# Kernel optimization log

Hardware: AMD Instinct MI355X
Metric: run time of the kernel (lower is better)

## Reference

```python
import jax, jax.numpy as jnp
import numpy as np

IN_DIM = 1024
OUT_DIM = 1024
BATCH = 256
NUM_OBJS = 100


def setup_inputs() -> dict:
    key = jax.random.key(0)
    k1, k2, k3, k4, k5 = jax.random.split(key, 5)
    stdv = 1.0 / np.sqrt(OUT_DIM)
    feature = jax.random.normal(k1, (BATCH, NUM_OBJS, IN_DIM), dtype=jnp.float32)
    graph = jax.random.randint(k2, (BATCH, NUM_OBJS, NUM_OBJS), 0, 2, dtype=jnp.int32)
    weight = jax.random.uniform(k3, (IN_DIM, OUT_DIM), dtype=jnp.float32, minval=-stdv, maxval=stdv)
    # DotProduct(in_dim, in_dim, out_dim): project both operands to hidden dim, batched dot product
    wq = jax.random.uniform(k4, (IN_DIM, OUT_DIM), dtype=jnp.float32, minval=-stdv, maxval=stdv)
    wk = jax.random.uniform(k5, (IN_DIM, OUT_DIM), dtype=jnp.float32, minval=-stdv, maxval=stdv)
    return {"feature": feature, "graph": graph, "weight": weight, "wq": wq, "wk": wk}


def reference(feature, graph, weight, wq, wk):
    # output = feature @ W                              [B, N, out_dim]
    output = jnp.einsum("bni,io->bno", feature, weight)
    # alpha = dot_product(feature, feature)             [B, N, N]
    q = jnp.einsum("bni,io->bno", feature, wq)
    k = jnp.einsum("bni,io->bno", feature, wk)
    alpha = jnp.einsum("bno,bmo->bnm", q, k)
    # relu scores, mask by adjacency, softmax over dim=1
    alpha = jnp.maximum(alpha, 0.0) * (graph != 0).astype(alpha.dtype)
    alpha = jax.nn.softmax(alpha, axis=1)
    # aggregate
    return jnp.einsum("bnm,bmo->bno", alpha, output)
```

## Files before the change

### kernel.cpp

```cpp
#include <hip/hip_runtime.h>
#include <cstdint>
#include <cstddef>

#define NOBJ 100

typedef __attribute__((ext_vector_type(8))) short short8;
typedef __attribute__((ext_vector_type(4))) float f32x4;

typedef const __attribute__((address_space(1))) void* gas_cptr;
typedef __attribute__((address_space(3))) void* las_ptr;

__device__ __forceinline__ void gload_lds16(const void* g, void* l) {
  __builtin_amdgcn_global_load_lds((gas_cptr)g, (las_ptr)l, 16, 0, 0);
}

__device__ __forceinline__ unsigned short bf16_rtne(float x) {
  unsigned u = __builtin_bit_cast(unsigned, x);
  unsigned r = u + 0x7FFFu + ((u >> 16) & 1u);
  return (unsigned short)(r >> 16);
}
__device__ __forceinline__ float bf16_to_f32(unsigned short h) {
  unsigned u = ((unsigned)h) << 16;
  return __builtin_bit_cast(float, u);
}

__global__ __launch_bounds__(256)
void split_ew(const float* __restrict__ in, unsigned short* __restrict__ hi,
              unsigned short* __restrict__ lo, long long n8) {
  for (long long u = (long long)blockIdx.x * 256 + threadIdx.x; u < n8;
       u += (long long)gridDim.x * 256) {
    const float4* p = (const float4*)(in + u * 8);
    float4 v0 = p[0], v1 = p[1];
    float x[8] = {v0.x, v0.y, v0.z, v0.w, v1.x, v1.y, v1.z, v1.w};
    unsigned h[8], l[8];
#pragma unroll
    for (int j = 0; j < 8; ++j) {
      h[j] = bf16_rtne(x[j]);
      l[j] = bf16_rtne(x[j] - bf16_to_f32((unsigned short)h[j]));
    }
    uint4 hv, lv;
    hv.x = h[0] | (h[1] << 16); hv.y = h[2] | (h[3] << 16);
    hv.z = h[4] | (h[5] << 16); hv.w = h[6] | (h[7] << 16);
    lv.x = l[0] | (l[1] << 16); lv.y = l[2] | (l[3] << 16);
    lv.z = l[4] | (l[5] << 16); lv.w = l[6] | (l[7] << 16);
    *(uint4*)(hi + u * 8) = hv;
    *(uint4*)(lo + u * 8) = lv;
  }
}

__global__ __launch_bounds__(256)
void split_tr(const float* __restrict__ W, unsigned short* __restrict__ thi,
              unsigned short* __restrict__ tlo) {
  __shared__ float tile[32][33];
  const int r0 = blockIdx.y * 32, c0 = blockIdx.x * 32;
  const int tx = threadIdx.x & 31, ty = threadIdx.x >> 5;
  for (int rr = ty; rr < 32; rr += 8)
    tile[rr][tx] = W[(size_t)(r0 + rr) * 1024 + c0 + tx];
  __syncthreads();
  for (int cc = ty; cc < 32; cc += 8) {
    float x = tile[tx][cc];
    unsigned short h = bf16_rtne(x);
    unsigned short l = bf16_rtne(x - bf16_to_f32(h));
    size_t o = (size_t)(c0 + cc) * 1024 + r0 + tx;
    thi[o] = h;
    tlo[o] = l;
  }
}

template<int EPI>
__global__ __launch_bounds__(256)
void gemm_mfma3(const unsigned short* __restrict__ Ah, const unsigned short* __restrict__ Al,
                const unsigned short* __restrict__ Bh, const unsigned short* __restrict__ Bl,
                unsigned short* __restrict__ Ch, unsigned short* __restrict__ Cl,
                int M, int N, int K) {
  __shared__ unsigned short s_ah[4096], s_al[4096], s_bh[4096], s_bl[4096];
  const int t = threadIdx.x;
  const int wid = t >> 6, lane = t & 63;
  const int wr = wid >> 1, wc = wid & 1;
  const int lrow = lane & 15, q = lane >> 4;
  const int m0 = blockIdx.y * 128, n0 = blockIdx.x * 128;

  const int srow = t >> 2;
  const int skch = (t & 3) ^ ((t >> 3) & 3);
  const unsigned short* gAh = Ah + (size_t)(m0 + srow) * K + skch * 8;
  const unsigned short* gAl = Al + (size_t)(m0 + srow) * K + skch * 8;
  const unsigned short* gBh = Bh + (size_t)(n0 + srow) * K + skch * 8;
  const unsigned short* gBl = Bl + (size_t)(n0 + srow) * K + skch * 8;
  const size_t rstep = (size_t)64 * K;
  unsigned short* dA0  = &s_ah[wid * 512];
  unsigned short* dA1  = &s_ah[wid * 512 + 2048];
  unsigned short* dAl0 = &s_al[wid * 512];
  unsigned short* dAl1 = &s_al[wid * 512 + 2048];
  unsigned short* dB0  = &s_bh[wid * 512];
  unsigned short* dB1  = &s_bh[wid * 512 + 2048];
  unsigned short* dBl0 = &s_bl[wid * 512];
  unsigned short* dBl1 = &s_bl[wid * 512 + 2048];

  const int fq = (q ^ ((lrow >> 1) & 3)) * 8;

  f32x4 acc[4][4];
#pragma unroll
  for (int i = 0; i < 4; ++i)
#pragma unroll
    for (int j = 0; j < 4; ++j) acc[i][j] = (f32x4){0.f, 0.f, 0.f, 0.f};

  for (int kc = 0; kc < K; kc += 32) {
    gload_lds16(gAh + kc, dA0);
    gload_lds16(gAh + kc + rstep, dA1);
    gload_lds16(gAl + kc, dAl0);
    gload_lds16(gAl + kc + rstep, dAl1);
    gload_lds16(gBh + kc, dB0);
    gload_lds16(gBh + kc + rstep, dB1);
    gload_lds16(gBl + kc, dBl0);
    gload_lds16(gBl + kc + rstep, dBl1);
    __syncthreads();

    short8 a_h[4], a_l[4];
#pragma unroll
    for (int i = 0; i < 4; ++i) {
      const int ra = (wr * 64 + i * 16 + lrow) * 32 + fq;
      a_h[i] = *(const short8*)&s_ah[ra];
      a_l[i] = *(const short8*)&s_al[ra];
    }
#pragma unroll
    for (int j = 0; j < 4; ++j) {
      const int rb = (wc * 64 + j * 16 + lrow) * 32 + fq;
      short8 b_h = *(const short8*)&s_bh[rb];
      short8 b_l = *(const short8*)&s_bl[rb];
#pragma unroll
      for (int i = 0; i < 4; ++i) {
        acc[i][j] = __builtin_amdgcn_mfma_f32_16x16x32_bf16(a_h[i], b_h, acc[i][j], 0, 0, 0);
        acc[i][j] = __builtin_amdgcn_mfma_f32_16x16x32_bf16(a_h[i], b_l, acc[i][j], 0, 0, 0);
        acc[i][j] = __builtin_amdgcn_mfma_f32_16x16x32_bf16(a_l[i], b_h, acc[i][j], 0, 0, 0);
      }
    }
    __syncthreads();
  }

#pragma unroll
  for (int i = 0; i < 4; ++i) {
    const int row0 = m0 + wr * 64 + i * 16 + q * 4;
#pragma unroll
    for (int j = 0; j < 4; ++j) {
      const int col = n0 + wc * 64 + j * 16 + lrow;
      unsigned short h[4];
#pragma unroll
      for (int r = 0; r < 4; ++r) h[r] = bf16_rtne(acc[i][j][r]);
      if (EPI == 0) {
#pragma unroll
        for (int r = 0; r < 4; ++r) {
          const size_t o = (size_t)(row0 + r) * N + col;
          Ch[o] = h[r];
          Cl[o] = bf16_rtne(acc[i][j][r] - bf16_to_f32(h[r]));
        }
      } else if (EPI == 1) {
        const unsigned bb = (unsigned)row0 / 100u;
        const unsigned ml = (unsigned)row0 - bb * 100u;
        uint2 hv;
        hv.x = (unsigned)h[0] | ((unsigned)h[1] << 16);
        hv.y = (unsigned)h[2] | ((unsigned)h[3] << 16);
        *(uint2*)(Ch + ((size_t)bb * 1024 + col) * 128 + ml) = hv;
      } else {
        unsigned short l[4];
#pragma unroll
        for (int r = 0; r < 4; ++r) l[r] = bf16_rtne(acc[i][j][r] - bf16_to_f32(h[r]));
        uint2 hv, lv;
        hv.x = (unsigned)h[0] | ((unsigned)h[1] << 16);
        hv.y = (unsigned)h[2] | ((unsigned)h[3] << 16);
        lv.x = (unsigned)l[0] | ((unsigned)l[1] << 16);
        lv.y = (unsigned)l[2] | ((unsigned)l[3] << 16);
        *(uint2*)(Ch + (size_t)col * 1024 + row0) = hv;
        *(uint2*)(Cl + (size_t)col * 1024 + row0) = lv;
      }
    }
  }
}

__global__ __launch_bounds__(256)
void attn_scores_mfma(const unsigned short* __restrict__ Qh, const unsigned short* __restrict__ Ql,
                      const unsigned short* __restrict__ Xh, const unsigned short* __restrict__ Xl,
                      const int* __restrict__ graph, float* __restrict__ S) {
  __shared__ unsigned short s_ah[4096], s_al[4096], s_bh[4096], s_bl[4096];
  __shared__ float s[NOBJ * NOBJ];
  const int t = threadIdx.x;
  const int wid = t >> 6, lane = t & 63;
  const int wr = wid >> 1, wc = wid & 1;
  const int lrow = lane & 15, q = lane >> 4;
  const int bb = blockIdx.x;

  const int srow = t >> 2;
  const int skch = (t & 3) ^ ((t >> 3) & 3);
  const int r0c = srow;
  const int r1c = (srow + 64) < NOBJ ? (srow + 64) : (NOBJ - 1);
  const size_t base = (size_t)bb * NOBJ * 1024;
  const unsigned short* gQh0 = Qh + base + (size_t)r0c * 1024 + skch * 8;
  const unsigned short* gQh1 = Qh + base + (size_t)r1c * 1024 + skch * 8;
  const unsigned short* gQl0 = Ql + base + (size_t)r0c * 1024 + skch * 8;
  const unsigned short* gQl1 = Ql + base + (size_t)r1c * 1024 + skch * 8;
  const unsigned short* gXh0 = Xh + base + (size_t)r0c * 1024 + skch * 8;
  const unsigned short* gXh1 = Xh + base + (size_t)r1c * 1024 + skch * 8;
  const unsigned short* gXl0 = Xl + base + (size_t)r0c * 1024 + skch * 8;
  const unsigned short* gXl1 = Xl + base + (size_t)r1c * 1024 + skch * 8;
  unsigned short* dA0  = &s_ah[wid * 512];
  unsigned short* dA1  = &s_ah[wid * 512 + 2048];
  unsigned short* dAl0 = &s_al[wid * 512];
  unsigned short* dAl1 = &s_al[wid * 512 + 2048];
  unsigned short* dB0  = &s_bh[wid * 512];
  unsigned short* dB1  = &s_bh[wid * 512 + 2048];
  unsigned short* dBl0 = &s_bl[wid * 512];
  unsigned short* dBl1 = &s_bl[wid * 512 + 2048];

  const int fq = (q ^ ((lrow >> 1) & 3)) * 8;

  f32x4 acc[4][4];
#pragma unroll
  for (int i = 0; i < 4; ++i)
#pragma unroll
    for (int j = 0; j < 4; ++j) acc[i][j] = (f32x4){0.f, 0.f, 0.f, 0.f};

  for (int kc = 0; kc < 1024; kc += 32) {
    gload_lds16(gQh0 + kc, dA0);
    gload_lds16(gQh1 + kc, dA1);
    gload_lds16(gQl0 + kc, dAl0);
    gload_lds16(gQl1 + kc, dAl1);
    gload_lds16(gXh0 + kc, dB0);
    gload_lds16(gXh1 + kc, dB1);
    gload_lds16(gXl0 + kc, dBl0);
    gload_lds16(gXl1 + kc, dBl1);
    __syncthreads();

    short8 a_h[4], a_l[4];
#pragma unroll
    for (int i = 0; i < 4; ++i) {
      const int ra = (wr * 64 + i * 16 + lrow) * 32 + fq;
      a_h[i] = *(const short8*)&s_ah[ra];
      a_l[i] = *(const short8*)&s_al[ra];
    }
#pragma unroll
    for (int j = 0; j < 4; ++j) {
      const int rb = (wc * 64 + j * 16 + lrow) * 32 + fq;
      short8 b_h = *(const short8*)&s_bh[rb];
      short8 b_l = *(const short8*)&s_bl[rb];
#pragma unroll
      for (int i = 0; i < 4; ++i) {
        acc[i][j] = __builtin_amdgcn_mfma_f32_16x16x32_bf16(a_h[i], b_h, acc[i][j], 0, 0, 0);
        acc[i][j] = __builtin_amdgcn_mfma_f32_16x16x32_bf16(a_h[i], b_l, acc[i][j], 0, 0, 0);
        acc[i][j] = __builtin_amdgcn_mfma_f32_16x16x32_bf16(a_l[i], b_h, acc[i][j], 0, 0, 0);
      }
    }
    __syncthreads();
  }

  const int* gb = graph + (size_t)bb * NOBJ * NOBJ;
#pragma unroll
  for (int i = 0; i < 4; ++i) {
    const int row0 = wr * 64 + i * 16 + q * 4;
#pragma unroll
    for (int j = 0; j < 4; ++j) {
      const int col = wc * 64 + j * 16 + lrow;
      if (col < NOBJ) {
#pragma unroll
        for (int r = 0; r < 4; ++r) {
          const int n = row0 + r;
          if (n < NOBJ) {
            float v = acc[i][j][r];
            v = v > 0.f ? v : 0.f;
            s[n * NOBJ + col] = (gb[n * NOBJ + col] != 0) ? v : 0.f;
          }
        }
      }
    }
  }
  __syncthreads();

  if (t < NOBJ) {
    const int m = t;
    float mx = 0.f;
    for (int n = 0; n < NOBJ; ++n) mx = fmaxf(mx, s[n * NOBJ + m]);
    float sum = 0.f;
    for (int n = 0; n < NOBJ; ++n) {
      const float e = expf(s[n * NOBJ + m] - mx);
      s[n * NOBJ + m] = e;
      sum += e;
    }
    const float inv = 1.f / sum;
    for (int n = 0; n < NOBJ; ++n) s[n * NOBJ + m] *= inv;
  }
  __syncthreads();

  float* Sb = S + (size_t)bb * NOBJ * NOBJ;
  for (int idx = t; idx < NOBJ * NOBJ; idx += 256) Sb[idx] = s[idx];
}

__global__ __launch_bounds__(256)
void attn_agg_mfma(const float* __restrict__ S, const unsigned short* __restrict__ opT,
                   float* __restrict__ out) {
  __shared__ unsigned short shi[128 * 128];
  __shared__ unsigned short slo[128 * 128];
  __shared__ unsigned short bt[64 * 128];
  const int t = threadIdx.x;
  const int wid = t >> 6, lane = t & 63;
  const int wr = wid >> 1, wc = wid & 1;
  const int lrow = lane & 15, q = lane >> 4;
  const int bb = blockIdx.y, o0 = blockIdx.x * 64;

#pragma unroll
  for (int p = 0; p < 4; ++p) {
    const int u = p * 256 + t;
    const int row = u >> 4, sl = u & 15;
    const int sp = sl ^ (row & 7);
    gload_lds16(opT + ((size_t)(bb * 1024 + o0 + row)) * 128 + sp * 8,
                bt + (p * 256 + wid * 64) * 8);
  }

  {
    unsigned* z1 = (unsigned*)shi;
    unsigned* z2 = (unsigned*)slo;
    for (int idx = t; idx < 8192; idx += 256) { z1[idx] = 0u; z2[idx] = 0u; }
  }
  __syncthreads();

  const float* Sb = S + (size_t)bb * NOBJ * NOBJ;
  for (int idx = t; idx < NOBJ * NOBJ / 4; idx += 256) {
    const float4 v = ((const float4*)Sb)[idx];
    const int lin = idx * 4, n = lin / NOBJ, m = lin - n * NOBJ;
    const float x[4] = {v.x, v.y, v.z, v.w};
    unsigned short h[4], l[4];
#pragma unroll
    for (int e = 0; e < 4; ++e) {
      h[e] = bf16_rtne(x[e]);
      l[e] = bf16_rtne(x[e] - bf16_to_f32(h[e]));
    }
    const int byte = ((n * 128 + m) * 2) ^ ((n & 7) << 4);
    uint2 hv, lv;
    hv.x = (unsigned)h[0] | ((unsigned)h[1] << 16);
    hv.y = (unsigned)h[2] | ((unsigned)h[3] << 16);
    lv.x = (unsigned)l[0] | ((unsigned)l[1] << 16);
    lv.y = (unsigned)l[2] | ((unsigned)l[3] << 16);
    *(uint2*)((char*)shi + byte) = hv;
    *(uint2*)((char*)slo + byte) = lv;
  }
  __syncthreads();

  f32x4 acc[4][2];
#pragma unroll
  for (int i = 0; i < 4; ++i)
#pragma unroll
    for (int j = 0; j < 2; ++j) acc[i][j] = (f32x4){0.f, 0.f, 0.f, 0.f};

#pragma unroll
  for (int ks = 0; ks < 4; ++ks) {
    short8 ah[4], al[4], bv[2];
#pragma unroll
    for (int i = 0; i < 4; ++i) {
      const int row = wr * 64 + i * 16 + lrow;
      const int byte = row * 256 + (((ks * 4 + q) ^ (row & 7)) * 16);
      ah[i] = *(const short8*)((char*)shi + byte);
      al[i] = *(const short8*)((char*)slo + byte);
    }
#pragma unroll
    for (int j = 0; j < 2; ++j) {
      const int brow = wc * 32 + j * 16 + lrow;
      const int byte = brow * 256 + (((ks * 4 + q) ^ (brow & 7)) * 16);
      bv[j] = *(const short8*)((char*)bt + byte);
    }
#pragma unroll
    for (int i = 0; i < 4; ++i)
#pragma unroll
      for (int j = 0; j < 2; ++j) {
        acc[i][j] = __builtin_amdgcn_mfma_f32_16x16x32_bf16(ah[i], bv[j], acc[i][j], 0, 0, 0);
        acc[i][j] = __builtin_amdgcn_mfma_f32_16x16x32_bf16(al[i], bv[j], acc[i][j], 0, 0, 0);
      }
  }

#pragma unroll
  for (int i = 0; i < 4; ++i) {
    const int row0 = wr * 64 + i * 16 + q * 4;
#pragma unroll
    for (int j = 0; j < 2; ++j) {
      const int col = o0 + wc * 32 + j * 16 + lrow;
#pragma unroll
      for (int r = 0; r < 4; ++r) {
        const int n = row0 + r;
        if (n < NOBJ)
          out[((size_t)bb * NOBJ + n) * 1024 + col] = acc[i][j][r];
      }
    }
  }
}

extern "C" void kernel_launch(void* const* d_in, const int* in_sizes, int n_in,
                              void* d_out, int out_size, void* d_ws, size_t ws_size,
                              hipStream_t stream) {
  const float* feature = (const float*)d_in[0];
  const int*   graph   = (const int*)  d_in[1];
  const float* weight  = (const float*)d_in[2];
  const float* wq      = (const float*)d_in[3];
  const float* wk      = (const float*)d_in[4];
  float* out = (float*)d_out;

  const size_t NF = (size_t)25600 * 1024;
  const size_t OPT = (size_t)256 * 1024 * 128;
  const size_t W1 = (size_t)1024 * 1024;
  const size_t need = (2 * NF + OPT + 8 * W1) * 2 + (size_t)2560000 * 4;
  if (ws_size < need) return;

  unsigned short* qkhi  = (unsigned short*)d_ws;
  unsigned short* qklo  = qkhi + NF;
  unsigned short* opT   = qklo + NF;
  unsigned short* wthi  = opT + OPT;
  unsigned short* wtlo  = wthi + W1;
  unsigned short* m1thi = wtlo + W1;
  unsigned short* m1tlo = m1thi + W1;
  unsigned short* wqhi  = m1tlo + W1;
  unsigned short* wqlo  = wqhi + W1;
  unsigned short* wkhi  = wqlo + W1;
  unsigned short* wklo  = wkhi + W1;
  float* S = (float*)(wklo + W1);
  unsigned short* xhi = (unsigned short*)d_out;
  unsigned short* xlo = xhi + NF;

  const dim3 blk(256);
  split_ew<<<4096, blk, 0, stream>>>(feature, xhi, xlo, (long long)(NF / 8));
  split_ew<<<512, blk, 0, stream>>>(wq, wqhi, wqlo, (long long)(W1 / 8));
  split_ew<<<512, blk, 0, stream>>>(wk, wkhi, wklo, (long long)(W1 / 8));
  split_tr<<<dim3(32, 32), blk, 0, stream>>>(weight, wthi, wtlo);
  gemm_mfma3<2><<<dim3(8, 8), blk, 0, stream>>>(wqhi, wqlo, wkhi, wklo,
                                                m1thi, m1tlo, 1024, 1024, 1024);
  gemm_mfma3<1><<<dim3(8, 200), blk, 0, stream>>>(xhi, xlo, wthi, wtlo,
                                                  opT, nullptr, 25600, 1024, 1024);
  gemm_mfma3<0><<<dim3(8, 200), blk, 0, stream>>>(xhi, xlo, m1thi, m1tlo,
                                                  qkhi, qklo, 25600, 1024, 1024);
  attn_scores_mfma<<<dim3(256), blk, 0, stream>>>(qkhi, qklo, xhi, xlo, graph, S);
  attn_agg_mfma<<<dim3(16, 256), blk, 0, stream>>>(S, opT, out);
}
```

Measured before the change: 794.6 us.

## Switch split-precision from bf16 to fp16, merge projection GEMMs, widen score blocks

Every hi/lo split and MFMA moves from bf16 to fp16, using the hardware float-to-half conversion in place of manual bit rounding. The two big projection GEMMs (feature@W and feature@M1) become one launch of 3200 workgroups with a remapped block order, so tiles that share the same feature rows sit on nearby workgroups. The attention-score kernel goes to 512 threads with 8 waves, covering the 100 rows in one tile instead of two overlapping 64-row loads. The cost is fp16's narrower exponent range, which could overflow or underflow for some inputs.

```diff
diff --git a/kernel.cpp b/kernel.cpp
--- a/kernel.cpp
+++ b/kernel.cpp
@@ -4,7 +4,7 @@
 
 #define NOBJ 100
 
-typedef __attribute__((ext_vector_type(8))) short short8;
+typedef __attribute__((ext_vector_type(8))) _Float16 half8;
 typedef __attribute__((ext_vector_type(4))) float f32x4;
 
 typedef const __attribute__((address_space(1))) void* gas_cptr;
@@ -14,14 +14,14 @@
   __builtin_amdgcn_global_load_lds((gas_cptr)g, (las_ptr)l, 16, 0, 0);
 }
 
-__device__ __forceinline__ unsigned short bf16_rtne(float x) {
-  unsigned u = __builtin_bit_cast(unsigned, x);
-  unsigned r = u + 0x7FFFu + ((u >> 16) & 1u);
-  return (unsigned short)(r >> 16);
-}
-__device__ __forceinline__ float bf16_to_f32(unsigned short h) {
-  unsigned u = ((unsigned)h) << 16;
-  return __builtin_bit_cast(float, u);
+__device__ __forceinline__ unsigned short f16h(float x) {
+  return __builtin_bit_cast(unsigned short, (_Float16)x);
+}
+__device__ __forceinline__ void f16split(float x, unsigned& h, unsigned& l) {
+  _Float16 hh = (_Float16)x;
+  _Float16 ll = (_Float16)(x - (float)hh);
+  h = (unsigned)__builtin_bit_cast(unsigned short, hh);
+  l = (unsigned)__builtin_bit_cast(unsigned short, ll);
 }
 
 __global__ __launch_bounds__(256)
@@ -34,10 +34,7 @@
     float x[8] = {v0.x, v0.y, v0.z, v0.w, v1.x, v1.y, v1.z, v1.w};
     unsigned h[8], l[8];
 #pragma unroll
-    for (int j = 0; j < 8; ++j) {
-      h[j] = bf16_rtne(x[j]);
-      l[j] = bf16_rtne(x[j] - bf16_to_f32((unsigned short)h[j]));
-    }
+    for (int j = 0; j < 8; ++j) f16split(x[j], h[j], l[j]);
     uint4 hv, lv;
     hv.x = h[0] | (h[1] << 16); hv.y = h[2] | (h[3] << 16);
     hv.z = h[4] | (h[5] << 16); hv.w = h[6] | (h[7] << 16);
@@ -59,20 +56,18 @@
   __syncthreads();
   for (int cc = ty; cc < 32; cc += 8) {
     float x = tile[tx][cc];
-    unsigned short h = bf16_rtne(x);
-    unsigned short l = bf16_rtne(x - bf16_to_f32(h));
+    unsigned h, l;
+    f16split(x, h, l);
     size_t o = (size_t)(c0 + cc) * 1024 + r0 + tx;
-    thi[o] = h;
-    tlo[o] = l;
-  }
-}
-
-template<int EPI>
+    thi[o] = (unsigned short)h;
+    tlo[o] = (unsigned short)l;
+  }
+}
+
 __global__ __launch_bounds__(256)
-void gemm_mfma3(const unsigned short* __restrict__ Ah, const unsigned short* __restrict__ Al,
-                const unsigned short* __restrict__ Bh, const unsigned short* __restrict__ Bl,
-                unsigned short* __restrict__ Ch, unsigned short* __restrict__ Cl,
-                int M, int N, int K) {
+void gemm_m1(const unsigned short* __restrict__ Ah, const unsigned short* __restrict__ Al,
+             const unsigned short* __restrict__ Bh, const unsigned short* __restrict__ Bl,
+             unsigned short* __restrict__ Th, unsigned short* __restrict__ Tl) {
   __shared__ unsigned short s_ah[4096], s_al[4096], s_bh[4096], s_bl[4096];
   const int t = threadIdx.x;
   const int wid = t >> 6, lane = t & 63;
@@ -82,11 +77,11 @@
 
   const int srow = t >> 2;
   const int skch = (t & 3) ^ ((t >> 3) & 3);
-  const unsigned short* gAh = Ah + (size_t)(m0 + srow) * K + skch * 8;
-  const unsigned short* gAl = Al + (size_t)(m0 + srow) * K + skch * 8;
-  const unsigned short* gBh = Bh + (size_t)(n0 + srow) * K + skch * 8;
-  const unsigned short* gBl = Bl + (size_t)(n0 + srow) * K + skch * 8;
-  const size_t rstep = (size_t)64 * K;
+  const unsigned short* gAh = Ah + (size_t)(m0 + srow) * 1024 + skch * 8;
+  const unsigned short* gAl = Al + (size_t)(m0 + srow) * 1024 + skch * 8;
+  const unsigned short* gBh = Bh + (size_t)(n0 + srow) * 1024 + skch * 8;
+  const unsigned short* gBl = Bl + (size_t)(n0 + srow) * 1024 + skch * 8;
+  const size_t rstep = (size_t)64 * 1024;
   unsigned short* dA0  = &s_ah[wid * 512];
   unsigned short* dA1  = &s_ah[wid * 512 + 2048];
   unsigned short* dAl0 = &s_al[wid * 512];
@@ -95,7 +90,6 @@
   unsigned short* dB1  = &s_bh[wid * 512 + 2048];
   unsigned short* dBl0 = &s_bl[wid * 512];
   unsigned short* dBl1 = &s_bl[wid * 512 + 2048];
-
   const int fq = (q ^ ((lrow >> 1) & 3)) * 8;
 
   f32x4 acc[4][4];
@@ -104,7 +98,7 @@
 #pragma unroll
     for (int j = 0; j < 4; ++j) acc[i][j] = (f32x4){0.f, 0.f, 0.f, 0.f};
 
-  for (int kc = 0; kc < K; kc += 32) {
+  for (int kc = 0; kc < 1024; kc += 32) {
     gload_lds16(gAh + kc, dA0);
     gload_lds16(gAh + kc + rstep, dA1);
     gload_lds16(gAl + kc, dAl0);
@@ -114,24 +108,23 @@
     gload_lds16(gBl + kc, dBl0);
     gload_lds16(gBl + kc + rstep, dBl1);
     __syncthreads();
-
-    short8 a_h[4], a_l[4];
+    half8 a_h[4], a_l[4];
 #pragma unroll
     for (int i = 0; i < 4; ++i) {
       const int ra = (wr * 64 + i * 16 + lrow) * 32 + fq;
-      a_h[i] = *(const short8*)&s_ah[ra];
-      a_l[i] = *(const short8*)&s_al[ra];
+      a_h[i] = *(const half8*)&s_ah[ra];
+      a_l[i] = *(const half8*)&s_al[ra];
     }
 #pragma unroll
     for (int j = 0; j < 4; ++j) {
       const int rb = (wc * 64 + j * 16 + lrow) * 32 + fq;
-      short8 b_h = *(const short8*)&s_bh[rb];
-      short8 b_l = *(const short8*)&s_bl[rb];
+      half8 b_h = *(const half8*)&s_bh[rb];
+      half8 b_l = *(const half8*)&s_bl[rb];
 #pragma unroll
       for (int i = 0; i < 4; ++i) {
-        acc[i][j] = __builtin_amdgcn_mfma_f32_16x16x32_bf16(a_h[i], b_h, acc[i][j], 0, 0, 0);
-        acc[i][j] = __builtin_amdgcn_mfma_f32_16x16x32_bf16(a_h[i], b_l, acc[i][j], 0, 0, 0);
-        acc[i][j] = __builtin_amdgcn_mfma_f32_16x16x32_bf16(a_l[i], b_h, acc[i][j], 0, 0, 0);
+        acc[i][j] = __builtin_amdgcn_mfma_f32_16x16x32_f16(a_h[i], b_h, acc[i][j], 0, 0, 0);
+        acc[i][j] = __builtin_amdgcn_mfma_f32_16x16x32_f16(a_h[i], b_l, acc[i][j], 0, 0, 0);
+        acc[i][j] = __builtin_amdgcn_mfma_f32_16x16x32_f16(a_l[i], b_h, acc[i][j], 0, 0, 0);
       }
     }
     __syncthreads();
@@ -143,64 +136,46 @@
 #pragma unroll
     for (int j = 0; j < 4; ++j) {
       const int col = n0 + wc * 64 + j * 16 + lrow;
-      unsigned short h[4];
-#pragma unroll
-      for (int r = 0; r < 4; ++r) h[r] = bf16_rtne(acc[i][j][r]);
-      if (EPI == 0) {
-#pragma unroll
-        for (int r = 0; r < 4; ++r) {
-          const size_t o = (size_t)(row0 + r) * N + col;
-          Ch[o] = h[r];
-          Cl[o] = bf16_rtne(acc[i][j][r] - bf16_to_f32(h[r]));
-        }
-      } else if (EPI == 1) {
-        const unsigned bb = (unsigned)row0 / 100u;
-        const unsigned ml = (unsigned)row0 - bb * 100u;
-        uint2 hv;
-        hv.x = (unsigned)h[0] | ((unsigned)h[1] << 16);
-        hv.y = (unsigned)h[2] | ((unsigned)h[3] << 16);
-        *(uint2*)(Ch + ((size_t)bb * 1024 + col) * 128 + ml) = hv;
-      } else {
-        unsigned short l[4];
-#pragma unroll
-        for (int r = 0; r < 4; ++r) l[r] = bf16_rtne(acc[i][j][r] - bf16_to_f32(h[r]));
-        uint2 hv, lv;
-        hv.x = (unsigned)h[0] | ((unsigned)h[1] << 16);
-        hv.y = (unsigned)h[2] | ((unsigned)h[3] << 16);
-        lv.x = (unsigned)l[0] | ((unsigned)l[1] << 16);
-        lv.y = (unsigned)l[2] | ((unsigned)l[3] << 16);
-        *(uint2*)(Ch + (size_t)col * 1024 + row0) = hv;
-        *(uint2*)(Cl + (size_t)col * 1024 + row0) = lv;
-      }
+      unsigned h[4], l[4];
+#pragma unroll
+      for (int r = 0; r < 4; ++r) f16split(acc[i][j][r], h[r], l[r]);
+      uint2 hv, lv;
+      hv.x = h[0] | (h[1] << 16); hv.y = h[2] | (h[3] << 16);
+      lv.x = l[0] | (l[1] << 16); lv.y = l[2] | (l[3] << 16);
+      *(uint2*)(Th + (size_t)col * 1024 + row0) = hv;
+      *(uint2*)(Tl + (size_t)col * 1024 + row0) = lv;
     }
   }
 }
 
 __global__ __launch_bounds__(256)
-void attn_scores_mfma(const unsigned short* __restrict__ Qh, const unsigned short* __restrict__ Ql,
-                      const unsigned short* __restrict__ Xh, const unsigned short* __restrict__ Xl,
-                      const int* __restrict__ graph, float* __restrict__ S) {
+void proj_gemm(const unsigned short* __restrict__ Ah, const unsigned short* __restrict__ Al,
+               const unsigned short* __restrict__ Wh, const unsigned short* __restrict__ Wl,
+               const unsigned short* __restrict__ Mh, const unsigned short* __restrict__ Ml,
+               unsigned short* __restrict__ opT, unsigned short* __restrict__ qkh,
+               unsigned short* __restrict__ qkl) {
   __shared__ unsigned short s_ah[4096], s_al[4096], s_bh[4096], s_bl[4096];
-  __shared__ float s[NOBJ * NOBJ];
   const int t = threadIdx.x;
   const int wid = t >> 6, lane = t & 63;
   const int wr = wid >> 1, wc = wid & 1;
   const int lrow = lane & 15, q = lane >> 4;
-  const int bb = blockIdx.x;
+
+  const int bid  = blockIdx.x;
+  const int wgid = (bid & 7) * 400 + (bid >> 3);
+  const int m0   = (wgid >> 4) * 128;
+  const int cb   = wgid & 15;
+  const bool isW = cb < 8;
+  const int n0   = (isW ? cb : cb - 8) * 128;
+  const unsigned short* Bh = isW ? Wh : Mh;
+  const unsigned short* Bl = isW ? Wl : Ml;
 
   const int srow = t >> 2;
   const int skch = (t & 3) ^ ((t >> 3) & 3);
-  const int r0c = srow;
-  const int r1c = (srow + 64) < NOBJ ? (srow + 64) : (NOBJ - 1);
-  const size_t base = (size_t)bb * NOBJ * 1024;
-  const unsigned short* gQh0 = Qh + base + (size_t)r0c * 1024 + skch * 8;
-  const unsigned short* gQh1 = Qh + base + (size_t)r1c * 1024 + skch * 8;
-  const unsigned short* gQl0 = Ql + base + (size_t)r0c * 1024 + skch * 8;
-  const unsigned short* gQl1 = Ql + base + (size_t)r1c * 1024 + skch * 8;
-  const unsigned short* gXh0 = Xh + base + (size_t)r0c * 1024 + skch * 8;
-  const unsigned short* gXh1 = Xh + base + (size_t)r1c * 1024 + skch * 8;
-  const unsigned short* gXl0 = Xl + base + (size_t)r0c * 1024 + skch * 8;
-  const unsigned short* gXl1 = Xl + base + (size_t)r1c * 1024 + skch * 8;
+  const unsigned short* gAh = Ah + (size_t)(m0 + srow) * 1024 + skch * 8;
+  const unsigned short* gAl = Al + (size_t)(m0 + srow) * 1024 + skch * 8;
+  const unsigned short* gBh = Bh + (size_t)(n0 + srow) * 1024 + skch * 8;
+  const unsigned short* gBl = Bl + (size_t)(n0 + srow) * 1024 + skch * 8;
+  const size_t rstep = (size_t)64 * 1024;
   unsigned short* dA0  = &s_ah[wid * 512];
   unsigned short* dA1  = &s_ah[wid * 512 + 2048];
   unsigned short* dAl0 = &s_al[wid * 512];
@@ -209,7 +184,6 @@
   unsigned short* dB1  = &s_bh[wid * 512 + 2048];
   unsigned short* dBl0 = &s_bl[wid * 512];
   unsigned short* dBl1 = &s_bl[wid * 512 + 2048];
-
   const int fq = (q ^ ((lrow >> 1) & 3)) * 8;
 
   f32x4 acc[4][4];
@@ -219,33 +193,123 @@
     for (int j = 0; j < 4; ++j) acc[i][j] = (f32x4){0.f, 0.f, 0.f, 0.f};
 
   for (int kc = 0; kc < 1024; kc += 32) {
-    gload_lds16(gQh0 + kc, dA0);
-    gload_lds16(gQh1 + kc, dA1);
-    gload_lds16(gQl0 + kc, dAl0);
-    gload_lds16(gQl1 + kc, dAl1);
-    gload_lds16(gXh0 + kc, dB0);
-    gload_lds16(gXh1 + kc, dB1);
-    gload_lds16(gXl0 + kc, dBl0);
-    gload_lds16(gXl1 + kc, dBl1);
-    __syncthreads();
-
-    short8 a_h[4], a_l[4];
+    gload_lds16(gAh + kc, dA0);
+    gload_lds16(gAh + kc + rstep, dA1);
+    gload_lds16(gAl + kc, dAl0);
+    gload_lds16(gAl + kc + rstep, dAl1);
+    gload_lds16(gBh + kc, dB0);
+    gload_lds16(gBh + kc + rstep, dB1);
+    gload_lds16(gBl + kc, dBl0);
+    gload_lds16(gBl + kc + rstep, dBl1);
+    __syncthreads();
+    half8 a_h[4], a_l[4];
 #pragma unroll
     for (int i = 0; i < 4; ++i) {
       const int ra = (wr * 64 + i * 16 + lrow) * 32 + fq;
-      a_h[i] = *(const short8*)&s_ah[ra];
-      a_l[i] = *(const short8*)&s_al[ra];
+      a_h[i] = *(const half8*)&s_ah[ra];
+      a_l[i] = *(const half8*)&s_al[ra];
     }
 #pragma unroll
     for (int j = 0; j < 4; ++j) {
       const int rb = (wc * 64 + j * 16 + lrow) * 32 + fq;
-      short8 b_h = *(const short8*)&s_bh[rb];
-      short8 b_l = *(const short8*)&s_bl[rb];
+      half8 b_h = *(const half8*)&s_bh[rb];
+      half8 b_l = *(const half8*)&s_bl[rb];
 #pragma unroll
       for (int i = 0; i < 4; ++i) {
-        acc[i][j] = __builtin_amdgcn_mfma_f32_16x16x32_bf16(a_h[i], b_h, acc[i][j], 0, 0, 0);
-        acc[i][j] = __builtin_amdgcn_mfma_f32_16x16x32_bf16(a_h[i], b_l, acc[i][j], 0, 0, 0);
-        acc[i][j] = __builtin_amdgcn_mfma_f32_16x16x32_bf16(a_l[i], b_h, acc[i][j], 0, 0, 0);
+        acc[i][j] = __builtin_amdgcn_mfma_f32_16x16x32_f16(a_h[i], b_h, acc[i][j], 0, 0, 0);
+        acc[i][j] = __builtin_amdgcn_mfma_f32_16x16x32_f16(a_h[i], b_l, acc[i][j], 0, 0, 0);
+        acc[i][j] = __builtin_amdgcn_mfma_f32_16x16x32_f16(a_l[i], b_h, acc[i][j], 0, 0, 0);
+      }
+    }
+    __syncthreads();
+  }
+
+#pragma unroll
+  for (int i = 0; i < 4; ++i) {
+    const int row0 = m0 + wr * 64 + i * 16 + q * 4;
+#pragma unroll
+    for (int j = 0; j < 4; ++j) {
+      const int col = n0 + wc * 64 + j * 16 + lrow;
+      if (isW) {
+        unsigned h[4];
+#pragma unroll
+        for (int r = 0; r < 4; ++r) h[r] = (unsigned)f16h(acc[i][j][r]);
+        const unsigned bb = (unsigned)row0 / 100u;
+        const unsigned ml = (unsigned)row0 - bb * 100u;
+        uint2 hv;
+        hv.x = h[0] | (h[1] << 16);
+        hv.y = h[2] | (h[3] << 16);
+        *(uint2*)(opT + ((size_t)bb * 1024 + col) * 128 + ml) = hv;
+      } else {
+        unsigned h[4], l[4];
+#pragma unroll
+        for (int r = 0; r < 4; ++r) f16split(acc[i][j][r], h[r], l[r]);
+#pragma unroll
+        for (int r = 0; r < 4; ++r) {
+          const size_t o = (size_t)(row0 + r) * 1024 + col;
+          qkh[o] = (unsigned short)h[r];
+          qkl[o] = (unsigned short)l[r];
+        }
+      }
+    }
+  }
+}
+
+__global__ __launch_bounds__(512)
+void attn_scores_mfma(const unsigned short* __restrict__ Qh, const unsigned short* __restrict__ Ql,
+                      const unsigned short* __restrict__ Xh, const unsigned short* __restrict__ Xl,
+                      const int* __restrict__ graph, float* __restrict__ S) {
+  __shared__ unsigned short s_ah[4096], s_al[4096], s_bh[4096], s_bl[4096];
+  __shared__ float s[NOBJ * NOBJ];
+  const int t = threadIdx.x;
+  const int wid = t >> 6, lane = t & 63;
+  const int wr = wid >> 2, wc = wid & 3;
+  const int lrow = lane & 15, q = lane >> 4;
+  const int bb = blockIdx.x;
+
+  const int srow = t >> 2;
+  const int rc   = srow < NOBJ ? srow : (NOBJ - 1);
+  const int skch = (t & 3) ^ ((t >> 3) & 3);
+  const size_t base = (size_t)bb * NOBJ * 1024;
+  const unsigned short* gQh = Qh + base + (size_t)rc * 1024 + skch * 8;
+  const unsigned short* gQl = Ql + base + (size_t)rc * 1024 + skch * 8;
+  const unsigned short* gXh = Xh + base + (size_t)rc * 1024 + skch * 8;
+  const unsigned short* gXl = Xl + base + (size_t)rc * 1024 + skch * 8;
+  unsigned short* dQh = &s_ah[wid * 512];
+  unsigned short* dQl = &s_al[wid * 512];
+  unsigned short* dXh = &s_bh[wid * 512];
+  unsigned short* dXl = &s_bl[wid * 512];
+  const int fq = (q ^ ((lrow >> 1) & 3)) * 8;
+
+  f32x4 acc[4][2];
+#pragma unroll
+  for (int i = 0; i < 4; ++i)
+#pragma unroll
+    for (int j = 0; j < 2; ++j) acc[i][j] = (f32x4){0.f, 0.f, 0.f, 0.f};
+
+  for (int kc = 0; kc < 1024; kc += 32) {
+    gload_lds16(gQh + kc, dQh);
+    gload_lds16(gQl + kc, dQl);
+    gload_lds16(gXh + kc, dXh);
+    gload_lds16(gXl + kc, dXl);
+    __syncthreads();
+    half8 a_h[4], a_l[4];
+#pragma unroll
+    for (int i = 0; i < 4; ++i) {
+      const int ra = (wr * 64 + i * 16 + lrow) * 32 + fq;
+      a_h[i] = *(const half8*)&s_ah[ra];
+      a_l[i] = *(const half8*)&s_al[ra];
+    }
+#pragma unroll
+    for (int j = 0; j < 2; ++j) {
+      const int rb = (wc * 32 + j * 16 + lrow) * 32 + fq;
+      half8 b_h = *(const half8*)&s_bh[rb];
+      half8 b_l = *(const half8*)&s_bl[rb];
+#pragma unroll
+      for (int i = 0; i < 4; ++i) {
+        acc[i][j] = __builtin_amdgcn_mfma_f32_16x16x32_f16(a_h[i], b_h, acc[i][j], 0, 0, 0);
+        acc[i][j] = __builtin_amdgcn_mfma_f32_16x16x32_f16(a_h[i], b_l, acc[i][j], 0, 0, 0);
+        acc[i][j] = __builtin_amdgcn_mfma_f32_16x16x32_f16(a_l[i], b_h, acc[i][j], 0, 0, 0);
       }
     }
     __syncthreads();
@@ -256,8 +320,8 @@
   for (int i = 0; i < 4; ++i) {
     const int row0 = wr * 64 + i * 16 + q * 4;
 #pragma unroll
-    for (int j = 0; j < 4; ++j) {
-      const int col = wc * 64 + j * 16 + lrow;
+    for (int j = 0; j < 2; ++j) {
+      const int col = wc * 32 + j * 16 + lrow;
       if (col < NOBJ) {
 #pragma unroll
         for (int r = 0; r < 4; ++r) {
@@ -289,7 +353,7 @@
   __syncthreads();
 
   float* Sb = S + (size_t)bb * NOBJ * NOBJ;
-  for (int idx = t; idx < NOBJ * NOBJ; idx += 256) Sb[idx] = s[idx];
+  for (int idx = t; idx < NOBJ * NOBJ; idx += 512) Sb[idx] = s[idx];
 }
 
 __global__ __launch_bounds__(256)
@@ -325,18 +389,13 @@
     const float4 v = ((const float4*)Sb)[idx];
     const int lin = idx * 4, n = lin / NOBJ, m = lin - n * NOBJ;
     const float x[4] = {v.x, v.y, v.z, v.w};
-    unsigned short h[4], l[4];
-#pragma unroll
-    for (int e = 0; e < 4; ++e) {
-      h[e] = bf16_rtne(x[e]);
-      l[e] = bf16_rtne(x[e] - bf16_to_f32(h[e]));
-    }
+    unsigned h[4], l[4];
+#pragma unroll
+    for (int e = 0; e < 4; ++e) f16split(x[e], h[e], l[e]);
     const int byte = ((n * 128 + m) * 2) ^ ((n & 7) << 4);
     uint2 hv, lv;
-    hv.x = (unsigned)h[0] | ((unsigned)h[1] << 16);
-    hv.y = (unsigned)h[2] | ((unsigned)h[3] << 16);
-    lv.x = (unsigned)l[0] | ((unsigned)l[1] << 16);
-    lv.y = (unsigned)l[2] | ((unsigned)l[3] << 16);
+    hv.x = h[0] | (h[1] << 16); hv.y = h[2] | (h[3] << 16);
+    lv.x = l[0] | (l[1] << 16); lv.y = l[2] | (l[3] << 16);
     *(uint2*)((char*)shi + byte) = hv;
     *(uint2*)((char*)slo + byte) = lv;
   }
@@ -350,26 +409,26 @@
 
 #pragma unroll
   for (int ks = 0; ks < 4; ++ks) {
-    short8 ah[4], al[4], bv[2];
+    half8 ah[4], al[4], bv[2];
 #pragma unroll
     for (int i = 0; i < 4; ++i) {
       const int row = wr * 64 + i * 16 + lrow;
       const int byte = row * 256 + (((ks * 4 + q) ^ (row & 7)) * 16);
-      ah[i] = *(const short8*)((char*)shi + byte);
-      al[i] = *(const short8*)((char*)slo + byte);
+      ah[i] = *(const half8*)((char*)shi + byte);
+      al[i] = *(const half8*)((char*)slo + byte);
     }
 #pragma unroll
     for (int j = 0; j < 2; ++j) {
       const int brow = wc * 32 + j * 16 + lrow;
       const int byte = brow * 256 + (((ks * 4 + q) ^ (brow & 7)) * 16);
-      bv[j] = *(const short8*)((char*)bt + byte);
+      bv[j] = *(const half8*)((char*)bt + byte);
     }
 #pragma unroll
     for (int i = 0; i < 4; ++i)
 #pragma unroll
       for (int j = 0; j < 2; ++j) {
-        acc[i][j] = __builtin_amdgcn_mfma_f32_16x16x32_bf16(ah[i], bv[j], acc[i][j], 0, 0, 0);
-        acc[i][j] = __builtin_amdgcn_mfma_f32_16x16x32_bf16(al[i], bv[j], acc[i][j], 0, 0, 0);
+        acc[i][j] = __builtin_amdgcn_mfma_f32_16x16x32_f16(ah[i], bv[j], acc[i][j], 0, 0, 0);
+        acc[i][j] = __builtin_amdgcn_mfma_f32_16x16x32_f16(al[i], bv[j], acc[i][j], 0, 0, 0);
       }
   }
 
@@ -425,12 +484,9 @@
   split_ew<<<512, blk, 0, stream>>>(wq, wqhi, wqlo, (long long)(W1 / 8));
   split_ew<<<512, blk, 0, stream>>>(wk, wkhi, wklo, (long long)(W1 / 8));
   split_tr<<<dim3(32, 32), blk, 0, stream>>>(weight, wthi, wtlo);
-  gemm_mfma3<2><<<dim3(8, 8), blk, 0, stream>>>(wqhi, wqlo, wkhi, wklo,
-                                                m1thi, m1tlo, 1024, 1024, 1024);
-  gemm_mfma3<1><<<dim3(8, 200), blk, 0, stream>>>(xhi, xlo, wthi, wtlo,
-                                                  opT, nullptr, 25600, 1024, 1024);
-  gemm_mfma3<0><<<dim3(8, 200), blk, 0, stream>>>(xhi, xlo, m1thi, m1tlo,
-                                                  qkhi, qklo, 25600, 1024, 1024);
-  attn_scores_mfma<<<dim3(256), blk, 0, stream>>>(qkhi, qklo, xhi, xlo, graph, S);
+  gemm_m1<<<dim3(8, 8), blk, 0, stream>>>(wqhi, wqlo, wkhi, wklo, m1thi, m1tlo);
+  proj_gemm<<<3200, blk, 0, stream>>>(xhi, xlo, wthi, wtlo, m1thi, m1tlo,
+                                      opT, qkhi, qklo);
+  attn_scores_mfma<<<dim3(256), dim3(512), 0, stream>>>(qkhi, qklo, xhi, xlo, graph, S);
   attn_agg_mfma<<<dim3(16, 256), blk, 0, stream>>>(S, opT, out);
 }
```

Measured after the change: 746.0 us. 6.1% less time.
